# Kernel tuning notes

Hardware: AMD Instinct MI355X
Metric: run time of the kernel (lower is better)

The kernel has to match this reference:

```python
import jax, jax.numpy as jnp
import numpy as np

N_HEADS = 12


def setup_inputs() -> dict:
    key = jax.random.key(0)
    ks = jax.random.split(key, 4)
    B, T, C = 1, 4096, 768
    x = jax.random.normal(ks[0], (B, T, C), dtype=jnp.float32)
    w_qkv = jax.random.normal(ks[1], (C, 3 * C), dtype=jnp.float32) * (C ** -0.5)
    b_qkv = jnp.zeros((3 * C,), dtype=jnp.float32)
    w_proj = jax.random.normal(ks[2], (C, C), dtype=jnp.float32) * (C ** -0.5)
    b_proj = jnp.zeros((C,), dtype=jnp.float32)
    return {"x": x, "w_qkv": w_qkv, "b_qkv": b_qkv, "w_proj": w_proj, "b_proj": b_proj}


def reference(x, w_qkv, b_qkv, w_proj, b_proj):
    B, T, C = x.shape
    H = N_HEADS
    hd = C // H
    qkv = x @ w_qkv + b_qkv                      # [B,T,3C]
    q, k, v = jnp.split(qkv, 3, axis=-1)
    # [B,H,T,hd]
    q = q.reshape(B, T, H, hd).transpose(0, 2, 1, 3)
    k = k.reshape(B, T, H, hd).transpose(0, 2, 1, 3)
    v = v.reshape(B, T, H, hd).transpose(0, 2, 1, 3)
    scale = 1.0 / jnp.sqrt(jnp.float32(hd))
    attn = jnp.einsum('bhqd,bhkd->bhqk', q, k) * scale  # [B,H,T,T]
    causal = jnp.tril(jnp.ones((T, T), dtype=bool))
    attn = jnp.where(causal, attn, jnp.float32(-jnp.inf))
    attn = jax.nn.softmax(attn, axis=-1)
    out = jnp.einsum('bhqk,bhkd->bhqd', attn, v)        # [B,H,T,hd]
    out = out.transpose(0, 2, 1, 3).reshape(B, T, C)
    return out @ w_proj + b_proj
```

## Files before the change

### kernel.cpp

```cpp
#include <hip/hip_runtime.h>
#include <hip/hip_bf16.h>


#define T_SEQ 4096
#define C_DIM 768
#define C3    2304
#define NH    12
#define HD    64

typedef __attribute__((ext_vector_type(8))) short bf16x8;
typedef __attribute__((ext_vector_type(4))) short bf16x4;
typedef __attribute__((ext_vector_type(4))) float f32x4;

__device__ inline unsigned short f2bf(float f) {
  union { float f; unsigned u; } v; v.f = f;
  unsigned r = v.u + 0x7fff + ((v.u >> 16) & 1);
  return (unsigned short)(r >> 16);
}
__device__ inline unsigned short f2bf_trunc(float f) {
  union { float f; unsigned u; } v; v.f = f;
  return (unsigned short)(v.u >> 16);
}

__device__ inline void gl2lds16(const void* g, void* l) {
  __builtin_amdgcn_global_load_lds(
      (const __attribute__((address_space(1))) unsigned int*)g,
      (__attribute__((address_space(3))) unsigned int*)l, 16, 0, 0);
}

#if __has_builtin(__builtin_amdgcn_exp2f)
#define EXP2F(x) __builtin_amdgcn_exp2f(x)
#else
#define EXP2F(x) exp2f(x)
#endif

#define NB_CONV  (T_SEQ * C_DIM / 2048)
#define NB_TQKV  ((C3 / 32) * (C_DIM / 32))
#define NB_TPROJ ((C_DIM / 32) * (C_DIM / 32))

__global__ __launch_bounds__(256) void prep_fused(
    const float* __restrict__ x, const float* __restrict__ w_qkv,
    const float* __restrict__ w_proj, unsigned short* __restrict__ xb,
    unsigned short* __restrict__ wqkvT, unsigned short* __restrict__ wprojT) {
  __shared__ float t[32][33];
  const int b = blockIdx.x;
  const int tid = threadIdx.x;

  if (b < NB_CONV) {
    int i = (b * 256 + tid) * 8;
    float4 v0 = *(const float4*)(x + i);
    float4 v1 = *(const float4*)(x + i + 4);
    unsigned short o[8] = {f2bf(v0.x), f2bf(v0.y), f2bf(v0.z), f2bf(v0.w),
                           f2bf(v1.x), f2bf(v1.y), f2bf(v1.z), f2bf(v1.w)};
    *(uint4*)(xb + i) = *(uint4*)o;
    return;
  }
  const float* in;
  unsigned short* outT;
  int R, Cc, bi;
  if (b < NB_CONV + NB_TQKV) {
    in = w_qkv; outT = wqkvT; R = C_DIM; Cc = C3; bi = b - NB_CONV;
  } else {
    in = w_proj; outT = wprojT; R = C_DIM; Cc = C_DIM; bi = b - NB_CONV - NB_TQKV;
  }
  const int tx = tid & 31, ty = tid >> 5;
  const int c0 = (bi % (Cc / 32)) * 32, r0 = (bi / (Cc / 32)) * 32;
#pragma unroll
  for (int i = 0; i < 4; ++i) {
    int r = ty + i * 8;
    t[r][tx] = in[(size_t)(r0 + r) * Cc + c0 + tx];
  }
  __syncthreads();
#pragma unroll
  for (int i = 0; i < 4; ++i) {
    int c = ty + i * 8;
    outT[(size_t)(c0 + c) * R + r0 + tx] = f2bf(t[tx][c]);
  }
}

__global__ __launch_bounds__(256) void gemm_qkv(
    const unsigned short* __restrict__ A, const unsigned short* __restrict__ Bt,
    const float* __restrict__ bias, unsigned short* __restrict__ Cq,
    unsigned short* __restrict__ vTp, int M, int N, int K) {
  __shared__ unsigned short As[128 * 64];
  __shared__ unsigned short Bs[128 * 64];
  const int tid = threadIdx.x;
  const int wave = tid >> 6, lane = tid & 63;
  const int lo = lane & 15, g8 = lane >> 4;
  const int lo7 = lo & 7;
  const int wm = wave >> 1, wn = wave & 1;
  const int bm = blockIdx.y * 128, bn = blockIdx.x * 128;
  const int drow8 = lane >> 3;
  const int dslot = (lane & 7) * 8;
  const int dsrc = ((lane & 7) ^ drow8) * 8;

  f32x4 acc[4][4];
#pragma unroll
  for (int mt = 0; mt < 4; ++mt)
#pragma unroll
    for (int nt = 0; nt < 4; ++nt) acc[mt][nt] = (f32x4){0.f, 0.f, 0.f, 0.f};

  const unsigned short* Abase = A + (size_t)bm * K;
  const unsigned short* Bbase = Bt + (size_t)bn * K;

  for (int k0 = 0; k0 < K; k0 += 64) {
    __syncthreads();
#pragma unroll
    for (int p = 0; p < 4; ++p) {
      const int r = p * 32 + wave * 8 + drow8;
      gl2lds16(Abase + (size_t)r * K + k0 + dsrc, As + r * 64 + dslot);
      gl2lds16(Bbase + (size_t)r * K + k0 + dsrc, Bs + r * 64 + dslot);
    }
    __syncthreads();

#pragma unroll
    for (int kk = 0; kk < 2; ++kk) {
      bf16x8 a[4], b[4];
#pragma unroll
      for (int mt = 0; mt < 4; ++mt)
        a[mt] = *(const bf16x8*)(
            As + (wm * 64 + mt * 16 + lo) * 64 + (((kk * 4 + g8) ^ lo7) * 8));
#pragma unroll
      for (int nt = 0; nt < 4; ++nt)
        b[nt] = *(const bf16x8*)(
            Bs + (wn * 64 + nt * 16 + lo) * 64 + (((kk * 4 + g8) ^ lo7) * 8));
#pragma unroll
      for (int mt = 0; mt < 4; ++mt)
#pragma unroll
        for (int nt = 0; nt < 4; ++nt)
          acc[mt][nt] = __builtin_amdgcn_mfma_f32_16x16x32_bf16(a[mt], b[nt], acc[mt][nt], 0, 0, 0);
    }
  }

  if (bn < 2 * C_DIM) {
    const float sc = (bn < C_DIM) ? 0.18033688011112042f : 1.0f;
#pragma unroll
    for (int nt = 0; nt < 4; ++nt) {
      const int n = bn + wn * 64 + nt * 16 + lo;
      const float bv = bias[n];
#pragma unroll
      for (int mt = 0; mt < 4; ++mt)
#pragma unroll
        for (int r = 0; r < 4; ++r) {
          const int m = bm + wm * 64 + mt * 16 + g8 * 4 + r;
          Cq[(size_t)m * C3 + n] = f2bf((acc[mt][nt][r] + bv) * sc);
        }
    }
  } else {
#pragma unroll
    for (int nt = 0; nt < 4; ++nt) {
      const int n = bn + wn * 64 + nt * 16 + lo;
      const float bv = bias[n];
      unsigned short* row = vTp + (size_t)(n - 2 * C_DIM) * T_SEQ;
#pragma unroll
      for (int mt = 0; mt < 4; ++mt) {
        const int mbase = (bm + wm * 64 + mt * 16 + g8 * 4) & ~31;
        bf16x4 o4;
#pragma unroll
        for (int r = 0; r < 4; ++r) o4[r] = (short)f2bf(acc[mt][nt][r] + bv);
        *(bf16x4*)(row + mbase + 8 * g8 + 4 * (mt & 1)) = o4;
      }
    }
  }
}

__global__ __launch_bounds__(256) void gemm_bt_mfma(
    const unsigned short* __restrict__ A, const unsigned short* __restrict__ Bt,
    const float* __restrict__ bias, float* __restrict__ C,
    int M, int N, int K) {
  __shared__ unsigned short As[128 * 64];
  __shared__ unsigned short Bs[128 * 64];
  const int tid = threadIdx.x;
  const int wave = tid >> 6, lane = tid & 63;
  const int lo = lane & 15, g8 = lane >> 4;
  const int lo7 = lo & 7;
  const int wm = wave >> 1, wn = wave & 1;
  const int bm = blockIdx.y * 128, bn = blockIdx.x * 128;
  const int drow8 = lane >> 3;
  const int dslot = (lane & 7) * 8;
  const int dsrc = ((lane & 7) ^ drow8) * 8;

  f32x4 acc[4][4];
#pragma unroll
  for (int mt = 0; mt < 4; ++mt)
#pragma unroll
    for (int nt = 0; nt < 4; ++nt) acc[mt][nt] = (f32x4){0.f, 0.f, 0.f, 0.f};

  const unsigned short* Abase = A + (size_t)bm * K;
  const unsigned short* Bbase = Bt + (size_t)bn * K;

  for (int k0 = 0; k0 < K; k0 += 64) {
    __syncthreads();
#pragma unroll
    for (int p = 0; p < 4; ++p) {
      const int r = p * 32 + wave * 8 + drow8;
      gl2lds16(Abase + (size_t)r * K + k0 + dsrc, As + r * 64 + dslot);
      gl2lds16(Bbase + (size_t)r * K + k0 + dsrc, Bs + r * 64 + dslot);
    }
    __syncthreads();

#pragma unroll
    for (int kk = 0; kk < 2; ++kk) {
      bf16x8 a[4], b[4];
#pragma unroll
      for (int mt = 0; mt < 4; ++mt)
        a[mt] = *(const bf16x8*)(
            As + (wm * 64 + mt * 16 + lo) * 64 + (((kk * 4 + g8) ^ lo7) * 8));
#pragma unroll
      for (int nt = 0; nt < 4; ++nt)
        b[nt] = *(const bf16x8*)(
            Bs + (wn * 64 + nt * 16 + lo) * 64 + (((kk * 4 + g8) ^ lo7) * 8));
#pragma unroll
      for (int mt = 0; mt < 4; ++mt)
#pragma unroll
        for (int nt = 0; nt < 4; ++nt)
          acc[mt][nt] = __builtin_amdgcn_mfma_f32_16x16x32_bf16(a[mt], b[nt], acc[mt][nt], 0, 0, 0);
    }
  }

#pragma unroll
  for (int nt = 0; nt < 4; ++nt) {
    const int n = bn + wn * 64 + nt * 16 + lo;
    const float bv = bias[n];
#pragma unroll
    for (int mt = 0; mt < 4; ++mt)
#pragma unroll
      for (int r = 0; r < 4; ++r) {
        const int m = bm + wm * 64 + mt * 16 + g8 * 4 + r;
        C[(size_t)m * N + n] = acc[mt][nt][r] + bv;
      }
  }
}

#define PO_SLOT ((size_t)NH * 32 * 128 * 64)
#define PL_SLOT ((size_t)NH * 32 * 128)
#define KSTEP   (64 * C3)

__global__ __launch_bounds__(256) void flash_attn_qb128(
    const unsigned short* __restrict__ qkv,
    const unsigned short* __restrict__ vTp,
    float* __restrict__ Po, float* __restrict__ Pl) {
  __shared__ unsigned short Ks[3][64 * 64];
  __shared__ unsigned short Vs[3][64 * 64];

  const int orig = blockIdx.x;
  const int xcd = orig & 7;
  const int o8 = orig >> 3;
  const int idx = ((xcd < 4) ? xcd * 95 : 380 + (xcd - 4) * 94) + o8;
  const int h = idx / 63;
  const int rem = idx - h * 63;
  int qt, c;
  if (rem < 30)      { qt = 22 + rem / 3;  c = rem % 3; }
  else if (rem < 52) { int r2 = rem - 30; qt = 11 + (r2 >> 1); c = r2 & 1; }
  else               { qt = rem - 52;      c = 0; }
  const int qt2 = 2 * qt;
  const int k0 = 22 * c;
  const int kmax = qt2 + 2;
  const int k1 = (k0 + 22 < kmax) ? (k0 + 22) : kmax;
  const int T = k1 - k0;

  const int tid = threadIdx.x;
  const int w = tid >> 6;
  const int lane = tid & 63;
  const int lo = lane & 15;
  const int g = lane >> 4;
  const int lo7 = lo & 7;

  const unsigned short* Kg = qkv + C_DIM + h * HD;
  const unsigned short* Vg = vTp + (size_t)(h * HD) * T_SEQ;

  const int drow = tid >> 3;
  const int dslot = (tid & 7) * 8;
  const int dsrc = ((tid & 7) ^ (drow & 7)) * 8;

  const int qw0 = w * 32 + lo;
  bf16x8 qb[2][2];
#pragma unroll
  for (int qh = 0; qh < 2; ++qh)
#pragma unroll
    for (int dh = 0; dh < 2; ++dh)
      qb[qh][dh] = *(const bf16x8*)(
          qkv + (size_t)(qt * 128 + qw0 + qh * 16) * C3 + h * HD + dh * 32 + g * 8);

  const unsigned short* pK0 = Kg + (size_t)k0 * KSTEP + (size_t)drow * C3 + dsrc;
  const unsigned short* pK1 = pK0 + (size_t)32 * C3;
  const unsigned short* pV0 = Vg + (size_t)drow * T_SEQ + k0 * 64 + dsrc;
  const unsigned short* pV1 = pV0 + (size_t)32 * T_SEQ;

  auto stage = [&](int buf) __attribute__((always_inline)) {
    gl2lds16(pK0, Ks[buf] + drow * 64 + dslot);
    gl2lds16(pK1, Ks[buf] + (32 + drow) * 64 + dslot);
    gl2lds16(pV0, Vs[buf] + drow * 64 + dslot);
    gl2lds16(pV1, Vs[buf] + (32 + drow) * 64 + dslot);
    pK0 += KSTEP; pK1 += KSTEP; pV0 += 64; pV1 += 64;
  };

  bf16x8 onesb;
#pragma unroll
  for (int e = 0; e < 8; ++e) onesb[e] = (short)0x3F80;

  stage(0);
  stage(1);
  asm volatile("s_waitcnt vmcnt(4)" ::: "memory");
  __builtin_amdgcn_s_barrier();

  f32x4 o_acc[2][4];
  f32x4 lacc[2];
#pragma unroll
  for (int qh = 0; qh < 2; ++qh) {
    lacc[qh] = (f32x4){0.f, 0.f, 0.f, 0.f};
#pragma unroll
    for (int dt = 0; dt < 4; ++dt) o_acc[qh][dt] = (f32x4){0.f, 0.f, 0.f, 0.f};
  }

  int ic = 0, iw = 2;
  int ktc = k0;
  for (int t = 0; t < T; ++t) {
    if (t + 2 < T) stage(iw);
    const unsigned short* Kc = Ks[ic];
    const unsigned short* Vc = Vs[ic];

    f32x4 st[2][4];
#pragma unroll
    for (int qh = 0; qh < 2; ++qh)
#pragma unroll
      for (int mt = 0; mt < 4; ++mt) st[qh][mt] = (f32x4){0.f, 0.f, 0.f, 0.f};
    __builtin_amdgcn_s_setprio(1);
#pragma unroll
    for (int mt = 0; mt < 4; ++mt)
#pragma unroll
      for (int dh = 0; dh < 2; ++dh) {
        bf16x8 a = *(const bf16x8*)(
            Kc + (mt * 16 + lo) * 64 + (((dh * 4 + g) ^ lo7) * 8));
#pragma unroll
        for (int qh = 0; qh < 2; ++qh)
          st[qh][mt] = __builtin_amdgcn_mfma_f32_16x16x32_bf16(
              a, qb[qh][dh], st[qh][mt], 0, 0, 0);
      }
    __builtin_amdgcn_s_setprio(0);

    if (ktc >= qt2) {
      const int mb = (ktc == qt2) ? 0 : 64;
#pragma unroll
      for (int qh = 0; qh < 2; ++qh) {
        const int qr = qw0 + qh * 16;
#pragma unroll
        for (int mt = 0; mt < 4; ++mt)
#pragma unroll
          for (int r = 0; r < 4; ++r)
            if (mb + mt * 16 + g * 4 + r > qr) st[qh][mt][r] = -1e30f;
      }
    }

    bf16x8 pt[2][2];
#pragma unroll
    for (int qh = 0; qh < 2; ++qh)
#pragma unroll
      for (int kh = 0; kh < 2; ++kh)
#pragma unroll
        for (int jj = 0; jj < 4; ++jj) {
          float e0 = EXP2F(st[qh][kh * 2][jj]);
          float e1 = EXP2F(st[qh][kh * 2 + 1][jj]);
          pt[qh][kh][jj] = (short)f2bf_trunc(e0);
          pt[qh][kh][4 + jj] = (short)f2bf_trunc(e1);
        }

    __builtin_amdgcn_s_setprio(1);
#pragma unroll
    for (int qh = 0; qh < 2; ++qh) {
      lacc[qh] = __builtin_amdgcn_mfma_f32_16x16x32_bf16(onesb, pt[qh][0], lacc[qh], 0, 0, 0);
      lacc[qh] = __builtin_amdgcn_mfma_f32_16x16x32_bf16(onesb, pt[qh][1], lacc[qh], 0, 0, 0);
    }
#pragma unroll
    for (int dt = 0; dt < 4; ++dt)
#pragma unroll
      for (int kh = 0; kh < 2; ++kh) {
        bf16x8 av = *(const bf16x8*)(
            Vc + (dt * 16 + lo) * 64 + (((kh * 4 + g) ^ lo7) * 8));
#pragma unroll
        for (int qh = 0; qh < 2; ++qh)
          o_acc[qh][dt] = __builtin_amdgcn_mfma_f32_16x16x32_bf16(
              av, pt[qh][kh], o_acc[qh][dt], 0, 0, 0);
      }
    __builtin_amdgcn_s_setprio(0);

    if (t + 2 < T)
      asm volatile("s_waitcnt vmcnt(4)" ::: "memory");
    else
      asm volatile("s_waitcnt vmcnt(0)" ::: "memory");
    __builtin_amdgcn_s_barrier();

    ic = (ic == 2) ? 0 : ic + 1;
    iw = (iw == 2) ? 0 : iw + 1;
    ++ktc;
  }

  float* PoS = Po + (((size_t)c * NH + h) * 32 + qt) * (128 * 64);
#pragma unroll
  for (int qh = 0; qh < 2; ++qh)
#pragma unroll
    for (int dt = 0; dt < 4; ++dt)
      *(f32x4*)(PoS + (qw0 + qh * 16) * 64 + dt * 16 + g * 4) = o_acc[qh][dt];
  if (g == 0) {
    float* PlS = Pl + (((size_t)c * NH + h) * 32 + qt) * 128;
#pragma unroll
    for (int qh = 0; qh < 2; ++qh) PlS[qw0 + qh * 16] = lacc[qh][0];
  }
}

__global__ __launch_bounds__(256) void combine_qb128(
    const float* __restrict__ Po, const float* __restrict__ Pl,
    unsigned short* __restrict__ out) {
  const int bid = blockIdx.x;
  const int h = bid >> 5, qt = bid & 31;
  const int tid = threadIdx.x;
  const int q = tid >> 1;
  const int c0 = (tid & 1) * 32;
  const bool v1 = (qt >= 11);
  const bool v2 = (qt >= 22);
  const size_t base = (size_t)h * 32 + qt;
  const float* P0 = Po + base * (128 * 64) + q * 64 + c0;
  float l = Pl[base * 128 + q];
  if (v1) l += Pl[PL_SLOT + base * 128 + q];
  if (v2) l += Pl[2 * PL_SLOT + base * 128 + q];
  const float inv = 1.0f / l;
  unsigned short ob[32];
#pragma unroll
  for (int e = 0; e < 8; ++e) {
    f32x4 v = *(const f32x4*)(P0 + e * 4);
    if (v1) v += *(const f32x4*)(P0 + PO_SLOT + e * 4);
    if (v2) v += *(const f32x4*)(P0 + 2 * PO_SLOT + e * 4);
#pragma unroll
    for (int r = 0; r < 4; ++r) ob[e * 4 + r] = f2bf(v[r] * inv);
  }
  unsigned short* op = out + (size_t)(qt * 128 + q) * C_DIM + h * 64 + c0;
#pragma unroll
  for (int e2 = 0; e2 < 4; ++e2)
    *(uint4*)(op + e2 * 8) = *(uint4*)(ob + e2 * 8);
}

extern "C" void kernel_launch(void* const* d_in, const int* in_sizes, int n_in,
                              void* d_out, int out_size, void* d_ws, size_t ws_size,
                              hipStream_t stream) {
  const float* x      = (const float*)d_in[0];
  const float* w_qkv  = (const float*)d_in[1];
  const float* b_qkv  = (const float*)d_in[2];
  const float* w_proj = (const float*)d_in[3];
  const float* b_proj = (const float*)d_in[4];
  float* out = (float*)d_out;

  unsigned short* xb     = (unsigned short*)d_ws;
  unsigned short* wqkvT  = xb + (size_t)T_SEQ * C_DIM;
  unsigned short* wprojT = wqkvT + (size_t)C3 * C_DIM;
  unsigned short* qkv    = wprojT + (size_t)C_DIM * C_DIM;
  unsigned short* vTp    = qkv + (size_t)T_SEQ * C3;
  unsigned short* attnb  = vTp + (size_t)C_DIM * T_SEQ;
  float* Po = (float*)(attnb + (size_t)T_SEQ * C_DIM);
  float* Pl = Po + 3 * PO_SLOT;

  prep_fused<<<NB_CONV + NB_TQKV + NB_TPROJ, 256, 0, stream>>>(
      x, w_qkv, w_proj, xb, wqkvT, wprojT);

  gemm_qkv<<<dim3(C3 / 128, T_SEQ / 128), 256, 0, stream>>>(
      xb, wqkvT, b_qkv, qkv, vTp, T_SEQ, C3, C_DIM);

  flash_attn_qb128<<<756, 256, 0, stream>>>(qkv, vTp, Po, Pl);

  combine_qb128<<<NH * 32, 256, 0, stream>>>(Po, Pl, attnb);

  gemm_bt_mfma<<<dim3(C_DIM / 128, T_SEQ / 128), 256, 0, stream>>>(
      attnb, wprojT, b_proj, out, T_SEQ, C_DIM, C_DIM);
}
```

Measured before the change: 187.2 us.

## Split causal attention KV range into 12-tile chunks with heavy-first block ordering

Changes the flash-attention split-K decomposition from up to 3 chunks of 22 KV tiles to up to 6 chunks of 12 KV tiles, launching 1224 blocks instead of 756. Blocks are ordered so full-length 12-tile chunks run first and the shorter tail chunks run last, and partial results are stored in a packed per-head record layout. The combine kernel now loops over a variable number of partials. This is meant to balance the load across CUs and shorten the tail, at the cost of more partial-output traffic and more combine work. It also drops the XCD-aware block remapping and reuses the xb buffer for the attention output.

Result: no change. 187.1 us (-0.1%).

```diff
diff --git a/kernel.cpp b/kernel.cpp
--- a/kernel.cpp
+++ b/kernel.cpp
@@ -232,32 +232,45 @@
   }
 }
 
-#define PO_SLOT ((size_t)NH * 32 * 128 * 64)
-#define PL_SLOT ((size_t)NH * 32 * 128)
-#define KSTEP   (64 * C3)
-
-__global__ __launch_bounds__(256) void flash_attn_qb128(
+#define NREC   102
+#define PO_REC (128 * 64)
+#define KSTEP  (64 * C3)
+
+__global__ __launch_bounds__(256) void flash_attn_d12(
     const unsigned short* __restrict__ qkv,
     const unsigned short* __restrict__ vTp,
     float* __restrict__ Po, float* __restrict__ Pl) {
   __shared__ unsigned short Ks[3][64 * 64];
   __shared__ unsigned short Vs[3][64 * 64];
 
-  const int orig = blockIdx.x;
-  const int xcd = orig & 7;
-  const int o8 = orig >> 3;
-  const int idx = ((xcd < 4) ? xcd * 95 : 380 + (xcd - 4) * 94) + o8;
-  const int h = idx / 63;
-  const int rem = idx - h * 63;
-  int qt, c;
-  if (rem < 30)      { qt = 22 + rem / 3;  c = rem % 3; }
-  else if (rem < 52) { int r2 = rem - 30; qt = 11 + (r2 >> 1); c = r2 & 1; }
-  else               { qt = rem - 52;      c = 0; }
+  const int u = blockIdx.x;
+  int h, qt, c;
+  if (u < 900) {
+    h = u / 75;
+    const int w = u % 75;
+    if (w < 15)      { qt = 29 + w / 5;          c = w % 5; }
+    else if (w < 39) { const int r = w - 15; qt = 23 + r / 4; c = r % 4; }
+    else if (w < 57) { const int r = w - 39; qt = 17 + r / 3; c = r % 3; }
+    else if (w < 69) { const int r = w - 57; qt = 11 + r / 2; c = r % 2; }
+    else             { qt = 5 + (w - 69);        c = 0; }
+  } else {
+    const int v = u - 900;
+    int m, r;
+    if (v < 60)       { m = 5; r = v; }
+    else if (v < 120) { m = 4; r = v - 60; }
+    else if (v < 180) { m = 3; r = v - 120; }
+    else if (v < 252) { m = 2; r = v - 180; }
+    else              { m = 1; r = v - 252; }
+    const int per = (m >= 3) ? 5 : 6;
+    h = r / per;
+    qt = (m - 1) + 6 * (r % per);
+    c = (qt + 1) / 6;
+  }
+  const int n = 2 * qt + 2;
+  const int k0 = 12 * c;
+  const int T = (n - k0 < 12) ? (n - k0) : 12;
   const int qt2 = 2 * qt;
-  const int k0 = 22 * c;
-  const int kmax = qt2 + 2;
-  const int k1 = (k0 + 22 < kmax) ? (k0 + 22) : kmax;
-  const int T = k1 - k0;
+  const int rec = c * (35 - 3 * c) + (qt - 6 * c);
 
   const int tid = threadIdx.x;
   const int w = tid >> 6;
@@ -395,20 +408,20 @@
     ++ktc;
   }
 
-  float* PoS = Po + (((size_t)c * NH + h) * 32 + qt) * (128 * 64);
+  float* PoS = Po + ((size_t)h * NREC + rec) * PO_REC;
 #pragma unroll
   for (int qh = 0; qh < 2; ++qh)
 #pragma unroll
     for (int dt = 0; dt < 4; ++dt)
       *(f32x4*)(PoS + (qw0 + qh * 16) * 64 + dt * 16 + g * 4) = o_acc[qh][dt];
   if (g == 0) {
-    float* PlS = Pl + (((size_t)c * NH + h) * 32 + qt) * 128;
+    float* PlS = Pl + ((size_t)h * NREC + rec) * 128;
 #pragma unroll
     for (int qh = 0; qh < 2; ++qh) PlS[qw0 + qh * 16] = lacc[qh][0];
   }
 }
 
-__global__ __launch_bounds__(256) void combine_qb128(
+__global__ __launch_bounds__(256) void combine_d12(
     const float* __restrict__ Po, const float* __restrict__ Pl,
     unsigned short* __restrict__ out) {
   const int bid = blockIdx.x;
@@ -416,23 +429,25 @@
   const int tid = threadIdx.x;
   const int q = tid >> 1;
   const int c0 = (tid & 1) * 32;
-  const bool v1 = (qt >= 11);
-  const bool v2 = (qt >= 22);
-  const size_t base = (size_t)h * 32 + qt;
-  const float* P0 = Po + base * (128 * 64) + q * 64 + c0;
-  float l = Pl[base * 128 + q];
-  if (v1) l += Pl[PL_SLOT + base * 128 + q];
-  if (v2) l += Pl[2 * PL_SLOT + base * 128 + q];
+  const int cmax = qt / 6;
+  float l = 0.f;
+  f32x4 acc[8];
+#pragma unroll
+  for (int e = 0; e < 8; ++e) acc[e] = (f32x4){0.f, 0.f, 0.f, 0.f};
+  for (int c = 0; c <= cmax; ++c) {
+    const int rec = c * (35 - 3 * c) + (qt - 6 * c);
+    const size_t base = (size_t)h * NREC + rec;
+    l += Pl[base * 128 + q];
+    const float* P = Po + base * PO_REC + q * 64 + c0;
+#pragma unroll
+    for (int e = 0; e < 8; ++e) acc[e] += *(const f32x4*)(P + e * 4);
+  }
   const float inv = 1.0f / l;
   unsigned short ob[32];
 #pragma unroll
-  for (int e = 0; e < 8; ++e) {
-    f32x4 v = *(const f32x4*)(P0 + e * 4);
-    if (v1) v += *(const f32x4*)(P0 + PO_SLOT + e * 4);
-    if (v2) v += *(const f32x4*)(P0 + 2 * PO_SLOT + e * 4);
-#pragma unroll
-    for (int r = 0; r < 4; ++r) ob[e * 4 + r] = f2bf(v[r] * inv);
-  }
+  for (int e = 0; e < 8; ++e)
+#pragma unroll
+    for (int r = 0; r < 4; ++r) ob[e * 4 + r] = f2bf(acc[e][r] * inv);
   unsigned short* op = out + (size_t)(qt * 128 + q) * C_DIM + h * 64 + c0;
 #pragma unroll
   for (int e2 = 0; e2 < 4; ++e2)
@@ -454,9 +469,9 @@
   unsigned short* wprojT = wqkvT + (size_t)C3 * C_DIM;
   unsigned short* qkv    = wprojT + (size_t)C_DIM * C_DIM;
   unsigned short* vTp    = qkv + (size_t)T_SEQ * C3;
-  unsigned short* attnb  = vTp + (size_t)C_DIM * T_SEQ;
-  float* Po = (float*)(attnb + (size_t)T_SEQ * C_DIM);
-  float* Pl = Po + 3 * PO_SLOT;
+  unsigned short* attnb  = xb;
+  float* Po = (float*)(vTp + (size_t)C_DIM * T_SEQ);
+  float* Pl = Po + (size_t)NH * NREC * PO_REC;
 
   prep_fused<<<NB_CONV + NB_TQKV + NB_TPROJ, 256, 0, stream>>>(
       x, w_qkv, w_proj, xb, wqkvT, wprojT);
@@ -464,9 +479,9 @@
   gemm_qkv<<<dim3(C3 / 128, T_SEQ / 128), 256, 0, stream>>>(
       xb, wqkvT, b_qkv, qkv, vTp, T_SEQ, C3, C_DIM);
 
-  flash_attn_qb128<<<756, 256, 0, stream>>>(qkv, vTp, Po, Pl);
-
-  combine_qb128<<<NH * 32, 256, 0, stream>>>(Po, Pl, attnb);
+  flash_attn_d12<<<1224, 256, 0, stream>>>(qkv, vTp, Po, Pl);
+
+  combine_d12<<<NH * 32, 256, 0, stream>>>(Po, Pl, attnb);
 
   gemm_bt_mfma<<<dim3(C_DIM / 128, T_SEQ / 128), 256, 0, stream>>>(
       attnb, wprojT, b_proj, out, T_SEQ, C_DIM, C_DIM);
```
